# Kernel tuning notes

Hardware: AMD Instinct MI355X
Metric: run time of the kernel (lower is better)

Reference implementation:

```python
import jax, jax.numpy as jnp
import numpy as np

DIM = 96
HEADS = 4
HID = int(DIM * 2.66)  # 255, GDFN hidden width
B, H, W = 4, 128, 128


def _conv(x, w, b=None, groups=1):
    y = jax.lax.conv_general_dilated(x, w, (1, 1), 'SAME',
                                     dimension_numbers=('NCHW', 'OIHW', 'NCHW'),
                                     feature_group_count=groups)
    return y if b is None else y + b[None, :, None, None]


def _ln(x, w, b):
    # WithBias LayerNorm over channel dim (per pixel), biased variance, eps=1e-5
    mu = x.mean(1, keepdims=True)
    var = ((x - mu) ** 2).mean(1, keepdims=True)
    return (x - mu) / jnp.sqrt(var + 1e-5) * w[None, :, None, None] + b[None, :, None, None]


def _l2norm(x):
    # torch F.normalize(dim=-1): x / max(||x||_2, 1e-12)
    return x / jnp.maximum(jnp.linalg.norm(x, axis=-1, keepdims=True), 1e-12)


def _gelu(x):
    return jax.nn.gelu(x, approximate=False)


def setup_inputs() -> dict:
    key = jax.random.key(0)
    ks = iter(jax.random.split(key, 32))
    nrm = lambda shp, s=0.02: jax.random.normal(next(ks), shp, dtype=jnp.float32) * s
    d, h2 = DIM, HID
    inp = {
        'x': jax.random.normal(next(ks), (B, DIM, H, W), dtype=jnp.float32),
        # L_conv: 3x3(d->d,+b) GELU 1x1(d->1,+b)
        'Lc_w1': nrm((d, d, 3, 3)), 'Lc_b1': jnp.zeros((d,), jnp.float32),
        'Lc_w2': nrm((1, d, 1, 1)), 'Lc_b2': jnp.zeros((1,), jnp.float32),
        # R_conv: 3x3(d->d,+b) GELU 1x1(d->3,+b)
        'Rc_w1': nrm((d, d, 3, 3)), 'Rc_b1': jnp.zeros((d,), jnp.float32),
        'Rc_w2': nrm((3, d, 1, 1)), 'Rc_b2': jnp.zeros((3,), jnp.float32),
        # L_rein: 3x3(1->d,+b) GELU ; R_rein: 3x3(3->d,+b)
        'Lr_w': nrm((d, 1, 3, 3)), 'Lr_b': jnp.zeros((d,), jnp.float32),
        'Rr_w': nrm((d, 3, 3, 3)), 'Rr_b': jnp.zeros((d,), jnp.float32),
        # LayerNorms (WithBias)
        'n1_w': jnp.ones((d,), jnp.float32), 'n1_b': jnp.zeros((d,), jnp.float32),
        'nL_w': jnp.ones((d,), jnp.float32), 'nL_b': jnp.zeros((d,), jnp.float32),
        'n2_w': jnp.ones((d,), jnp.float32), 'n2_b': jnp.zeros((d,), jnp.float32),
        # Illum_Attention (bias=False)
        'temp': jnp.ones((HEADS, 1, 1), jnp.float32),
        'q_w': nrm((d, d, 1, 1)),
        'qd_w': nrm((d, d, 3, 3)),          # q_dwconv is a FULL 3x3 conv (no groups)
        'kv_w': nrm((2 * d, d, 1, 1)),
        'kvd_w': nrm((2 * d, 1, 3, 3)),     # depthwise, groups=2*dim
        'po_w': nrm((d, d, 1, 1)),
        # FeedForward (bias=False); NOTE: 'dwconv' here is a FULL 3x3 conv
        'pi_w': nrm((h2, d, 1, 1)),
        'fdw_w': nrm((h2, h2, 3, 3)),
        'fpo_w': nrm((d, h2, 1, 1)),
    }
    return inp


def reference(x, Lc_w1, Lc_b1, Lc_w2, Lc_b2, Rc_w1, Rc_b1, Rc_w2, Rc_b2,
              Lr_w, Lr_b, Rr_w, Rr_b, n1_w, n1_b, nL_w, nL_b, n2_w, n2_b,
              temp, q_w, qd_w, kv_w, kvd_w, po_w, pi_w, fdw_w, fpo_w):
    b, c, h, w = x.shape
    # Retinex decomposition heads
    L = _conv(_gelu(_conv(x, Lc_w1, Lc_b1)), Lc_w2, Lc_b2)   # [b,1,h,w]
    R = _conv(_gelu(_conv(x, Rc_w1, Rc_b1)), Rc_w2, Rc_b2)   # [b,3,h,w]
    L_rein = _gelu(_conv(jax.lax.stop_gradient(L), Lr_w, Lr_b))  # detach in torch
    R_rein = _conv(jax.lax.stop_gradient(R), Rr_w, Rr_b)
    # Illum_Guided_TransformerBlock: x = x + attn(norm1(x), normL(illum))
    xn = _ln(x, n1_w, n1_b)
    ill = _ln(L_rein, nL_w, nL_b)
    q = _conv(_conv(ill, q_w), qd_w)
    kv = _conv(_conv(xn, kv_w), kvd_w, groups=2 * c)
    k, v = jnp.split(kv, 2, axis=1)
    ch, hw = c // HEADS, h * w
    heads = lambda t: t.reshape(b, HEADS, ch, hw)
    qh, kh, vh = _l2norm(heads(q)), _l2norm(heads(k)), heads(v)
    # channel-wise attention: [b,heads,ch,ch]
    attn = jax.nn.softmax(jnp.einsum('bhci,bhdi->bhcd', qh, kh) * temp[None], axis=-1)
    out = jnp.einsum('bhcd,bhdi->bhci', attn, vh).reshape(b, c, h, w)
    x = x + _conv(out, po_w)
    # x = x + ffn(norm2(x))
    x2 = _ln(x, n2_w, n2_b)
    x = x + _conv(_gelu(_conv(_conv(x2, pi_w), fdw_w)), fpo_w)
    x = x + R_rein
    return (x, L, R)
```

## Files before the change

kernel.cpp:

```cpp
#include <hip/hip_runtime.h>

#define HWsz 16384
#define Wd 128

typedef unsigned short ushortT;
typedef unsigned int uintT;
typedef __attribute__((ext_vector_type(8))) short short8v;
typedef __attribute__((ext_vector_type(4))) float f32x4;
typedef __attribute__((ext_vector_type(16))) float f32x16;
typedef __attribute__((ext_vector_type(4))) unsigned short ushort4v;

__device__ __forceinline__ float gelu_f(float x){
    return 0.5f * x * (1.0f + erff(x * 0.70710678118654752f));
}
__device__ __forceinline__ ushortT f2b(float f){
    union { float f; uintT u; } v; v.f = f;
    uintT r = v.u + 0x7FFFu + ((v.u >> 16) & 1u);
    return (ushortT)(r >> 16);
}
__device__ __forceinline__ float b2f(ushortT u){
    union { uintT u; float f; } v; v.u = ((uintT)u) << 16; return v.f;
}

__device__ __forceinline__ void pack3_one(int e, const float* __restrict__ w,
    ushortT* __restrict__ outp, int cout, int cin, int BN, int NCH)
{
    int j = e & 7; int r = e >> 3;
    int ocl = r % BN; r /= BN;
    int kg  = r & 3;  r >>= 2;
    int tap = r % 9;  r /= 9;
    int ch  = r % NCH;
    int nt  = r / NCH;
    int ci = ch*32 + kg*8 + j;
    int oc = nt*BN + ocl;
    float v = (oc < cout && ci < cin) ? w[((size_t)oc*cin + ci)*9 + tap] : 0.f;
    outp[e] = f2b(v);
}
__device__ __forceinline__ void pack1_one(int e, const float* __restrict__ w,
    ushortT* __restrict__ outp, int cout, int cin, int BN, int NCH)
{
    int j = e & 7; int r = e >> 3;
    int ocl = r % BN; r /= BN;
    int kg  = r & 3;  r >>= 2;
    int ch  = r % NCH;
    int nt  = r / NCH;
    int ci = ch*32 + kg*8 + j;
    int oc = nt*BN + ocl;
    float v = (oc < cout && ci < cin) ? w[(size_t)oc*cin + ci] : 0.f;
    outp[e] = f2b(v);
}
__global__ __launch_bounds__(256) void pack_all_kernel(
    const float* Lc, const float* Rc, const float* Qd, const float* Fd,
    const float* Q1, const float* KV1, const float* PI1, const float* FPO1,
    ushortT* dL, ushortT* dR, ushortT* dQ, ushortT* dF,
    ushortT* dq0, ushortT* dkv, ushortT* dpi, ushortT* dfpo)
{
    int e = blockIdx.x*256 + threadIdx.x;
    if      (e < 82944)  pack3_one(e,        Lc, dL, 96, 96, 48, 3);
    else if (e < 165888) pack3_one(e-82944,  Rc, dR, 96, 96, 48, 3);
    else if (e < 248832) pack3_one(e-165888, Qd, dQ, 96, 96, 32, 3);
    else if (e < 838656) pack3_one(e-248832, Fd, dF, 255,255, 64, 8);
    else if (e < 847872) pack1_one(e-838656, Q1, dq0, 96, 96, 96, 3);
    else if (e < 866304) pack1_one(e-847872, KV1,dkv, 192,96, 48, 3);
    else if (e < 890880) pack1_one(e-866304, PI1,dpi, 255,96, 64, 3);
    else if (e < 915456) pack1_one(e-890880, FPO1,dfpo,96,255, 96, 8);
}

__global__ __launch_bounds__(256) void tonhwc_kernel(
    const float* __restrict__ in, ushortT* __restrict__ outp)
{
    const int p = blockIdx.x*256 + threadIdx.x;
    const int b = blockIdx.y;
    const float* ip = in + (size_t)b*96*HWsz + p;
    ushortT* op = outp + ((size_t)b*HWsz + p)*96;
#pragma unroll
    for (int g=0; g<12; g++){
        float v[8];
#pragma unroll
        for (int c=0;c<8;c++) v[c] = ip[(size_t)(g*8+c)*HWsz];
        uint4 pk;
        pk.x = (uintT)f2b(v[0]) | ((uintT)f2b(v[1])<<16);
        pk.y = (uintT)f2b(v[2]) | ((uintT)f2b(v[3])<<16);
        pk.z = (uintT)f2b(v[4]) | ((uintT)f2b(v[5])<<16);
        pk.w = (uintT)f2b(v[6]) | ((uintT)f2b(v[7])<<16);
        *(uint4*)(op + g*8) = pk;
    }
}

template<int NG, int NCH, int ACT, int TWOOUT>
__global__ __launch_bounds__(256,2) void conv3x3_v2(
    const ushortT* __restrict__ inh,
    const ushortT* __restrict__ wpk1, const ushortT* __restrict__ wpk2,
    const float* __restrict__ bias1, const float* __restrict__ bias2,
    ushortT* __restrict__ out1, ushortT* __restrict__ out2,
    int cout, int ocpad)
{
    constexpr int BN = NG*16;
    constexpr int Cpad = NCH*32;
    __shared__ __align__(16) ushortT As[4*180*8];

    const int tid = threadIdx.x;
    const int l   = tid & 63;
    const int wv  = tid >> 6;
    const int l15 = l & 15;
    const int kg  = l >> 4;
    const int tix = blockIdx.x & 7, tiy = blockIdx.x >> 3;
    const int b   = blockIdx.z;
    const int x0 = tix*16, y0 = tiy*8;

    const ushortT* wpk; const float* bias; ushortT* outp; int nt;
    if (TWOOUT){
        wpk  = (wv >= 2) ? wpk2 : wpk1;
        bias = (wv >= 2) ? bias2 : bias1;
        outp = (wv >= 2) ? out2 : out1;
        nt = wv & 1;
    } else { wpk = wpk1; bias = bias1; outp = out1; nt = wv; }
    const int ocbase = nt*BN;

    f32x4 acc[8][NG];
#pragma unroll
    for (int m=0;m<8;m++)
#pragma unroll
        for (int n=0;n<NG;n++) acc[m][n] = (f32x4){0.f,0.f,0.f,0.f};

    const ushortT* inb = inh + (size_t)b*HWsz*Cpad;

    for (int ch=0; ch<NCH; ch++){
        __syncthreads();
#pragma unroll
        for (int g=0; g<4; g++){
            int p = tid;
            if (p < 180){
                int hy = p/18, hx = p - hy*18;
                int gy = y0 + hy - 1, gx = x0 + hx - 1;
                uint4 v; v.x=0u; v.y=0u; v.z=0u; v.w=0u;
                if ((unsigned)gy < 128u && (unsigned)gx < 128u)
                    v = *(const uint4*)(inb + (size_t)(gy*Wd+gx)*Cpad + ch*32 + g*8);
                *(uint4*)(As + (g*180+p)*8) = v;
            }
        }
        __syncthreads();
        const ushortT* wch = wpk + (size_t)(nt*NCH + ch)*(9*4*BN*8);
#pragma unroll
        for (int tp=0; tp<9; tp++){
            const int dy = tp/3, dx = tp - dy*3;
            short8v bf[NG];
#pragma unroll
            for (int n=0;n<NG;n++)
                bf[n] = *(const short8v*)(wch + ((size_t)(tp*4 + kg)*BN + n*16 + l15)*8);
#pragma unroll
            for (int mg=0;mg<8;mg++){
                short8v a = *(const short8v*)(As + (kg*180 + (mg+dy)*18 + l15+dx)*8);
#pragma unroll
                for (int n=0;n<NG;n++)
                    acc[mg][n] = __builtin_amdgcn_mfma_f32_16x16x32_bf16(a, bf[n], acc[mg][n], 0,0,0);
            }
        }
    }
    __syncthreads();
    ushortT* Ts = As + wv*1024;
#pragma unroll
    for (int mg=0;mg<8;mg++){
        int gy = y0 + mg;
        ushortT* orow = outp + ((size_t)b*HWsz + gy*Wd + x0)*ocpad + ocbase;
#pragma unroll
        for (int n=0;n<NG;n++){
            int ocl = n*16 + l15;
            int oc  = ocbase + ocl;
            float bs = (bias && oc < cout) ? bias[oc] : 0.f;
#pragma unroll
            for (int j=0;j<4;j++){
                int pxj = kg*4 + j;
                float r = 0.f;
                if (oc < cout){ r = acc[mg][n][j] + bs; if (ACT) r = gelu_f(r); }
                int seg = ((ocl>>3) + pxj) & 7;
                Ts[pxj*64 + seg*8 + (ocl&7)] = f2b(r);
            }
        }
#pragma unroll
        for (int ps=0; ps < (BN+31)/32; ps++){
            int rpx = l & 15;
            int rs  = (l>>4) + ps*4;
            if (rs*8 < BN){
                int pseg = (rs + rpx) & 7;
                short8v v = *(const short8v*)(Ts + rpx*64 + pseg*8);
                *(short8v*)(orow + (size_t)rpx*ocpad + rs*8) = v;
            }
        }
    }
}

template<int NGW, int NCH>
__global__ __launch_bounds__(256) void gemm1x1_v2(
    const ushortT* __restrict__ inh, const ushortT* __restrict__ wpk,
    ushortT* __restrict__ outp, int cout, int ocpad)
{
    constexpr int BN = NGW*16;
    constexpr int Cpad = NCH*32;
    __shared__ __align__(16) ushortT Ts[4*16*64];

    const int tid = threadIdx.x;
    const int l = tid & 63, wv = tid >> 6, l15 = l & 15, kg = l >> 4;
    const int p0 = blockIdx.x*64;
    const int b  = blockIdx.z;
    const int nt = wv, ocbase = wv*BN;
    const ushortT* inb = inh + (size_t)b*HWsz*Cpad;

    f32x4 acc[4][NGW];
#pragma unroll
    for (int m=0;m<4;m++)
#pragma unroll
        for (int n=0;n<NGW;n++) acc[m][n] = (f32x4){0.f,0.f,0.f,0.f};

#pragma unroll
    for (int ch=0; ch<NCH; ch++){
        short8v a[4], bw[NGW];
#pragma unroll
        for (int mg=0; mg<4; mg++)
            a[mg] = *(const short8v*)(inb + (size_t)(p0 + mg*16 + l15)*Cpad + ch*32 + kg*8);
#pragma unroll
        for (int n=0;n<NGW;n++)
            bw[n] = *(const short8v*)(wpk + (((size_t)(nt*NCH + ch)*4 + kg)*BN + n*16 + l15)*8);
#pragma unroll
        for (int mg=0;mg<4;mg++)
#pragma unroll
            for (int n=0;n<NGW;n++)
                acc[mg][n] = __builtin_amdgcn_mfma_f32_16x16x32_bf16(a[mg], bw[n], acc[mg][n], 0,0,0);
    }
    ushortT* Tw = Ts + wv*1024;
#pragma unroll
    for (int mg=0;mg<4;mg++){
        ushortT* orow = outp + ((size_t)b*HWsz + p0 + mg*16)*ocpad + ocbase;
#pragma unroll
        for (int n=0;n<NGW;n++){
            int ocl = n*16 + l15;
            int oc  = ocbase + ocl;
#pragma unroll
            for (int j=0;j<4;j++){
                int pxj = kg*4 + j;
                float r = (oc < cout) ? acc[mg][n][j] : 0.f;
                int seg = ((ocl>>3) + pxj) & 7;
                Tw[pxj*64 + seg*8 + (ocl&7)] = f2b(r);
            }
        }
#pragma unroll
        for (int ps=0; ps < (BN+31)/32; ps++){
            int rpx = l & 15;
            int rs  = (l>>4) + ps*4;
            if (rs*8 < BN){
                int pseg = (rs + rpx) & 7;
                short8v v = *(const short8v*)(Tw + rpx*64 + pseg*8);
                *(short8v*)(orow + (size_t)rpx*ocpad + rs*8) = v;
            }
        }
    }
}

template<int NG, int NCH, int ACT, int OMODE, int NSPLIT, int XMAP>
__global__ __launch_bounds__(256,4) void conv3x3_mfma(
    const ushortT* __restrict__ inh,
    const ushortT* __restrict__ wpk1, const ushortT* __restrict__ wpk2,
    const float* __restrict__ bias1, const float* __restrict__ bias2,
    void* __restrict__ out1, void* __restrict__ out2,
    int cout, int ocpad)
{
    constexpr int BN = NG*16;
    constexpr int Cpad = NCH*32;
    __shared__ __align__(16) ushortT As[4*324*8];

    const int tid = threadIdx.x;
    const int l   = tid & 63;
    const int wv  = tid >> 6;
    const int l15 = l & 15;
    const int kg  = l >> 4;
    int tile = blockIdx.x, nt = blockIdx.y, b = blockIdx.z;
    const int tix = tile & 7, tiy = tile >> 3;

    const ushortT* wpk = wpk1; const float* bias = bias1; void* outv = out1;
    if (NSPLIT > 0 && nt >= NSPLIT){ nt -= NSPLIT; wpk = wpk2; bias = bias2; outv = out2; }

    f32x4 acc[4][NG];
#pragma unroll
    for (int m=0;m<4;m++)
#pragma unroll
        for (int n=0;n<NG;n++) acc[m][n] = (f32x4){0.f,0.f,0.f,0.f};

    const ushortT* inb = inh + (size_t)b*HWsz*Cpad;

    for (int ch=0; ch<NCH; ch++){
        __syncthreads();
#pragma unroll
        for (int g=0; g<4; g++){
            for (int p=tid; p<324; p+=256){
                int hy = p/18, hx = p - hy*18;
                int gy = tiy*16 + hy - 1, gx = tix*16 + hx - 1;
                uint4 v; v.x=0u; v.y=0u; v.z=0u; v.w=0u;
                if ((unsigned)gy < 128u && (unsigned)gx < 128u)
                    v = *(const uint4*)(inb + (size_t)(gy*Wd+gx)*Cpad + ch*32 + g*8);
                *(uint4*)(As + (g*324+p)*8) = v;
            }
        }
        __syncthreads();
        const ushortT* wch = wpk + (size_t)(nt*NCH + ch)*(9*4*BN*8);
#pragma unroll
        for (int tp=0; tp<9; tp++){
            const int dy = tp/3, dx = tp - dy*3;
            short8v a[4], bf[NG];
#pragma unroll
            for (int mg=0; mg<4; mg++){
                int p = (wv*4 + mg + dy)*18 + l15 + dx;
                a[mg] = *(const short8v*)(As + (kg*324 + p)*8);
            }
#pragma unroll
            for (int n=0;n<NG;n++)
                bf[n] = *(const short8v*)(wch + ((size_t)(tp*4 + kg)*BN + n*16 + l15)*8);
#pragma unroll
            for (int mg=0;mg<4;mg++)
#pragma unroll
                for (int n=0;n<NG;n++)
                    acc[mg][n] = __builtin_amdgcn_mfma_f32_16x16x32_bf16(a[mg], bf[n], acc[mg][n], 0,0,0);
        }
    }
    if (OMODE == 2){
        ushortT* out = (ushortT*)outv;
#pragma unroll
        for (int n=0;n<NG;n++){
            int oc = nt*BN + n*16 + l15;
            if (oc < cout){
                float bs = bias ? bias[oc] : 0.f;
#pragma unroll
                for (int mg=0;mg<4;mg++){
                    int gy = tiy*16 + wv*4 + mg;
                    int gx = tix*16 + kg*4;
                    ushort4v pk;
#pragma unroll
                    for (int j=0;j<4;j++){
                        float r = acc[mg][n][j] + bs;
                        if (ACT) r = gelu_f(r);
                        pk[j] = f2b(r);
                    }
                    *(ushort4v*)(out + ((size_t)b*cout + oc)*HWsz + gy*Wd + gx) = pk;
                }
            }
        }
    }
}

template<int NG, int NCH, int RES, int OMODE, int XMAP>
__global__ __launch_bounds__(256) void gemm1x1_mfma(
    const ushortT* __restrict__ inh, const ushortT* __restrict__ wpk, int wstride_z,
    const float* __restrict__ res1, const ushortT* __restrict__ res2b,
    void* __restrict__ outv, int cout, int ocpad)
{
    constexpr int BN = NG*16;
    constexpr int Cpad = NCH*32;
    constexpr int LSTR = (BN <= 64) ? 64 : 128;
    constexpr int MASK = LSTR/8 - 1;
    __shared__ __align__(16) ushortT TsS[(OMODE==1) ? 4*16*LSTR : 16];

    const int tid = threadIdx.x;
    const int l = tid & 63, wv = tid >> 6, l15 = l & 15, kg = l >> 4;
    int chunk = blockIdx.x, nt = blockIdx.y, b = blockIdx.z;
    const int p0 = chunk*256 + wv*64;
    const ushortT* inb = inh + (size_t)b*HWsz*Cpad;
    const ushortT* wp  = wpk + (size_t)b*wstride_z;

    f32x4 acc[4][NG];
#pragma unroll
    for (int m=0;m<4;m++)
#pragma unroll
        for (int n=0;n<NG;n++) acc[m][n] = (f32x4){0.f,0.f,0.f,0.f};

#pragma unroll
    for (int ch=0; ch<NCH; ch++){
        short8v a[4], bw[NG];
#pragma unroll
        for (int mg=0; mg<4; mg++)
            a[mg] = *(const short8v*)(inb + (size_t)(p0 + mg*16 + l15)*Cpad + ch*32 + kg*8);
#pragma unroll
        for (int n=0;n<NG;n++)
            bw[n] = *(const short8v*)(wp + (((size_t)(nt*NCH + ch)*4 + kg)*BN + n*16 + l15)*8);
#pragma unroll
        for (int mg=0;mg<4;mg++)
#pragma unroll
            for (int n=0;n<NG;n++)
                acc[mg][n] = __builtin_amdgcn_mfma_f32_16x16x32_bf16(a[mg], bw[n], acc[mg][n], 0,0,0);
    }
    if (OMODE == 0){
        float* out = (float*)outv;
#pragma unroll
        for (int n=0;n<NG;n++){
            int oc = nt*BN + n*16 + l15;
            if (oc < cout){
#pragma unroll
                for (int mg=0;mg<4;mg++){
                    int pix = p0 + mg*16 + kg*4;
                    size_t idx = ((size_t)b*cout + oc)*HWsz + pix;
                    float4 r;
                    r.x = acc[mg][n][0]; r.y = acc[mg][n][1];
                    r.z = acc[mg][n][2]; r.w = acc[mg][n][3];
                    if (RES>=1){ float4 q = *(const float4*)(res1+idx); r.x+=q.x;r.y+=q.y;r.z+=q.z;r.w+=q.w; }
                    if (RES>=2){
                        ushort4v q = *(const ushort4v*)(res2b+idx);
                        r.x+=b2f(q[0]); r.y+=b2f(q[1]); r.z+=b2f(q[2]); r.w+=b2f(q[3]);
                    }
                    *(float4*)(out + idx) = r;
                }
            }
        }
    } else {
        ushortT* outp = (ushortT*)outv;
        ushortT* Ts = TsS + wv*(16*LSTR);
#pragma unroll
        for (int mg=0;mg<4;mg++){
            ushortT* orow = outp + ((size_t)b*HWsz + p0 + mg*16)*ocpad + nt*BN;
#pragma unroll
            for (int n=0;n<NG;n++){
                int ocl = n*16 + l15;
                int oc  = nt*BN + ocl;
#pragma unroll
                for (int j=0;j<4;j++){
                    int pxj = kg*4 + j;
                    float r = (oc < cout) ? acc[mg][n][j] : 0.f;
                    int seg = ((ocl>>3) + pxj) & MASK;
                    Ts[pxj*LSTR + seg*8 + (ocl&7)] = f2b(r);
                }
            }
#pragma unroll
            for (int ps=0; ps < (BN+31)/32; ps++){
                int rpx = l & 15;
                int rs  = (l>>4) + ps*4;
                if (rs*8 < BN){
                    int pseg = (rs + rpx) & MASK;
                    short8v v = *(const short8v*)(Ts + rpx*LSTR + pseg*8);
                    *(short8v*)(orow + (size_t)rpx*ocpad + rs*8) = v;
                }
            }
        }
    }
}

template<int NOUT>
__global__ __launch_bounds__(256) void head1x1_kernel(
    const ushortT* __restrict__ inh, const float* __restrict__ w,
    const float* __restrict__ bias, float* __restrict__ out)
{
    __shared__ float lw[NOUT*96];
    const int tid = threadIdx.x;
    for (int t=tid; t<NOUT*96; t+=256) lw[t] = w[t];
    __syncthreads();
    const int p = blockIdx.x*256 + tid;
    const int b = blockIdx.y;
    const ushortT* ip = inh + ((size_t)b*HWsz + p)*96;
    float v[96];
#pragma unroll
    for (int g=0; g<12; g++){
        short8v s = *(const short8v*)(ip + g*8);
#pragma unroll
        for (int i=0;i<8;i++) v[g*8+i] = b2f((ushortT)s[i]);
    }
#pragma unroll
    for (int oc=0; oc<NOUT; oc++){
        float acc = bias[oc];
#pragma unroll
        for (int c=0;c<96;c++) acc += v[c]*lw[oc*96+c];
        out[((size_t)b*NOUT + oc)*HWsz + p] = acc;
    }
}

__global__ __launch_bounds__(256) void lrein_ln_kernel(
    const float* __restrict__ L, const float* __restrict__ w,
    const float* __restrict__ bias, const float* __restrict__ lnw,
    const float* __restrict__ lnb, ushortT* __restrict__ outh)
{
    __shared__ float sw[864], sb[96], sn1[96], sn2[96];
    const int tid = threadIdx.x;
    for (int t=tid; t<864; t+=256) sw[t] = w[t];
    if (tid < 96){ sb[tid]=bias[tid]; sn1[tid]=lnw[tid]; sn2[tid]=lnb[tid]; }
    __syncthreads();
    const int p = blockIdx.x*256 + tid;
    const int b = blockIdx.y;
    const int y = p>>7, x = p&127;
    const float* ib = L + (size_t)b*HWsz;
    float win[9];
#pragma unroll
    for (int dy=0;dy<3;dy++)
#pragma unroll
        for (int dx=0;dx<3;dx++){
            int gy=y+dy-1, gx=x+dx-1;
            win[dy*3+dx] = ((unsigned)gy<128u && (unsigned)gx<128u) ? ib[gy*Wd+gx] : 0.f;
        }
    float v[96]; float s=0.f;
#pragma unroll
    for (int c=0;c<96;c++){
        float a = sb[c];
#pragma unroll
        for (int t=0;t<9;t++) a += win[t]*sw[c*9+t];
        a = gelu_f(a);
        v[c]=a; s+=a;
    }
    const float mu = s*(1.f/96.f);
    float s2=0.f;
#pragma unroll
    for (int c=0;c<96;c++){ float d=v[c]-mu; s2+=d*d; }
    const float inv = 1.f/sqrtf(s2*(1.f/96.f)+1e-5f);
    ushortT* op = outh + ((size_t)b*HWsz + p)*96;
#pragma unroll
    for (int g=0; g<12; g++){
        uint4 pk; uintT w4[4];
#pragma unroll
        for (int i=0;i<4;i++){
            float r0 = (v[g*8+2*i]-mu)*inv*sn1[g*8+2*i]+sn2[g*8+2*i];
            float r1 = (v[g*8+2*i+1]-mu)*inv*sn1[g*8+2*i+1]+sn2[g*8+2*i+1];
            w4[i] = (uintT)f2b(r0) | ((uintT)f2b(r1)<<16);
        }
        pk.x=w4[0]; pk.y=w4[1]; pk.z=w4[2]; pk.w=w4[3];
        *(uint4*)(op + g*8) = pk;
    }
}

__global__ __launch_bounds__(256) void ln_n2n_kernel(
    const float* __restrict__ in, const float* __restrict__ w,
    const float* __restrict__ bias, ushortT* __restrict__ outh)
{
    const int p = blockIdx.x*256+threadIdx.x;
    const int b = blockIdx.y;
    const float* ip = in + (size_t)b*96*HWsz + p;
    float v[96]; float s=0.f;
#pragma unroll
    for(int c=0;c<96;c++){ v[c]=ip[(size_t)c*HWsz]; s+=v[c]; }
    const float mu = s*(1.f/96.f);
    float s2=0.f;
#pragma unroll
    for(int c=0;c<96;c++){ float d=v[c]-mu; s2+=d*d; }
    const float inv = 1.f/sqrtf(s2*(1.f/96.f)+1e-5f);
    ushortT* op = outh + ((size_t)b*HWsz + p)*96;
#pragma unroll
    for (int g=0; g<12; g++){
        uint4 pk; uintT w4[4];
#pragma unroll
        for (int i=0;i<4;i++){
            float r0 = (v[g*8+2*i]-mu)*inv*w[g*8+2*i]+bias[g*8+2*i];
            float r1 = (v[g*8+2*i+1]-mu)*inv*w[g*8+2*i+1]+bias[g*8+2*i+1];
            w4[i] = (uintT)f2b(r0) | ((uintT)f2b(r1)<<16);
        }
        pk.x=w4[0]; pk.y=w4[1]; pk.z=w4[2]; pk.w=w4[3];
        *(uint4*)(op + g*8) = pk;
    }
}

__global__ __launch_bounds__(256) void conv3x3_rr_kernel(
    const float* __restrict__ in, const float* __restrict__ w,
    const float* __restrict__ bias, ushortT* __restrict__ out)
{
    __shared__ float sw[216], sb[8];
    const int oc0 = blockIdx.y*8;
    if (threadIdx.x < 216) sw[threadIdx.x] = w[(size_t)oc0*27 + threadIdx.x];
    if (threadIdx.x < 8)   sb[threadIdx.x] = bias[oc0 + threadIdx.x];
    __syncthreads();
    const int p = blockIdx.x*256+threadIdx.x;
    const int b = blockIdx.z;
    const int y=p>>7, x=p&127;
    const float* ib = in + (size_t)b*3*HWsz;
    float win[27];
#pragma unroll
    for (int ci=0;ci<3;ci++)
#pragma unroll
        for (int dy=0;dy<3;dy++)
#pragma unroll
            for (int dx=0;dx<3;dx++){
                int gy=y+dy-1, gx=x+dx-1;
                win[ci*9+dy*3+dx] = ((unsigned)gy<128u && (unsigned)gx<128u)
                    ? ib[(size_t)ci*HWsz + gy*Wd+gx] : 0.f;
            }
#pragma unroll
    for (int i=0;i<8;i++){
        float acc = sb[i];
#pragma unroll
        for (int t=0;t<27;t++) acc += win[t]*sw[i*27+t];
        out[((size_t)b*96 + oc0+i)*HWsz + p] = f2b(acc);
    }
}

__global__ __launch_bounds__(256) void dw_nhwc_kernel(
    const ushortT* __restrict__ inh, const float* __restrict__ w,
    ushortT* __restrict__ kout, ushortT* __restrict__ vouth)
{
    const int p = blockIdx.x*256+threadIdx.x;
    const int c0 = blockIdx.y*8;
    const int b = blockIdx.z;
    const int y=p>>7, x=p&127;
    float lw[72];
#pragma unroll
    for (int i=0;i<8;i++)
#pragma unroll
        for (int t=0;t<9;t++) lw[i*9+t] = w[(size_t)(c0+i)*9 + t];
    const ushortT* ib = inh + (size_t)b*HWsz*192;
    float acc[8];
#pragma unroll
    for (int i=0;i<8;i++) acc[i]=0.f;
#pragma unroll
    for(int dy=0;dy<3;dy++){
        int gy=y+dy-1;
        if((unsigned)gy<128u){
#pragma unroll
            for(int dx=0;dx<3;dx++){
                int gx=x+dx-1;
                if((unsigned)gx<128u){
                    short8v s = *(const short8v*)(ib + (size_t)(gy*Wd+gx)*192 + c0);
#pragma unroll
                    for (int i=0;i<8;i++) acc[i] += b2f((ushortT)s[i])*lw[i*9+dy*3+dx];
                }
            }
        }
    }
    if (c0 < 96){
#pragma unroll
        for (int i=0;i<8;i++)
            kout[((size_t)b*96 + c0+i)*HWsz + p] = f2b(acc[i]);
    } else {
        ushortT* op = vouth + ((size_t)b*HWsz + p)*96 + (c0-96);
        uint4 pk;
        pk.x = (uintT)f2b(acc[0]) | ((uintT)f2b(acc[1])<<16);
        pk.y = (uintT)f2b(acc[2]) | ((uintT)f2b(acc[3])<<16);
        pk.z = (uintT)f2b(acc[4]) | ((uintT)f2b(acc[5])<<16);
        pk.w = (uintT)f2b(acc[6]) | ((uintT)f2b(acc[7])<<16);
        *(uint4*)op = pk;
    }
}

__global__ __launch_bounds__(256) void rownorm_bf16_kernel(
    const ushortT* __restrict__ qb, const ushortT* __restrict__ kb,
    float* __restrict__ invqk)
{
    __shared__ float red[256];
    const int r = blockIdx.x;
    const ushortT* ip = (r < 384) ? (qb + (size_t)r*HWsz) : (kb + (size_t)(r-384)*HWsz);
    float s=0.f;
    const ushortT* tp = ip + threadIdx.x*64;
#pragma unroll
    for (int g=0; g<8; g++){
        short8v v = *(const short8v*)(tp + g*8);
#pragma unroll
        for (int i=0;i<8;i++){ float f = b2f((ushortT)v[i]); s += f*f; }
    }
    red[threadIdx.x]=s; __syncthreads();
    for(int st=128; st>0; st>>=1){
        if(threadIdx.x<st) red[threadIdx.x]+=red[threadIdx.x+st];
        __syncthreads();
    }
    if(threadIdx.x==0) invqk[r] = 1.f/fmaxf(sqrtf(red[0]), 1e-12f);
}

__global__ __launch_bounds__(256) void qk_mfma_kernel(
    const ushortT* __restrict__ qb, const ushortT* __restrict__ kb,
    float* __restrict__ part)
{
    const int tid = threadIdx.x;
    const int l = tid & 63, wv = tid >> 6;
    const int chunk = blockIdx.x*4 + wv;
    const int bh = blockIdx.y, b = bh>>2, h = bh&3;
    const int ch = min(l & 31, 23);
    const int kh = (l >> 5)*8;
    const ushortT* qp = qb + ((size_t)b*96 + h*24 + ch)*HWsz + chunk*512 + kh;
    const ushortT* kp = kb + ((size_t)b*96 + h*24 + ch)*HWsz + chunk*512 + kh;
    f32x16 acc;
#pragma unroll
    for (int r=0;r<16;r++) acc[r]=0.f;
    for (int ks=0; ks<32; ks++){
        short8v a  = *(const short8v*)(qp + ks*16);
        short8v bb = *(const short8v*)(kp + ks*16);
        acc = __builtin_amdgcn_mfma_f32_32x32x16_bf16(a, bb, acc, 0,0,0);
    }
    float* op = part + ((size_t)chunk*16 + bh)*1024;
    const int col = l & 31;
#pragma unroll
    for (int r=0;r<16;r++){
        int row = (r&3) + 8*(r>>2) + 4*(l>>5);
        op[row*32 + col] = acc[r];
    }
}

__global__ void qk_reduce_kernel(const float* __restrict__ part, float* __restrict__ out)
{
    int idx = blockIdx.x*256+threadIdx.x;
    float s=0.f;
    for(int c=0;c<32;c++) s += part[(size_t)c*16384 + idx];
    out[idx]=s;
}

__global__ __launch_bounds__(576) void softmax_kernel(
    const float* __restrict__ raw, const float* __restrict__ invq,
    const float* __restrict__ invk, const float* __restrict__ temp,
    float* __restrict__ attn)
{
    __shared__ float l[576];
    const int bh=blockIdx.x, b=bh>>2, h=bh&3;
    const int tid=threadIdx.x;
    const int i=tid/24, j=tid-i*24;
    l[tid] = raw[(size_t)bh*1024 + i*32 + j] * invq[b*96+h*24+i] * invk[b*96+h*24+j] * temp[h];
    __syncthreads();
    if(tid<24){
        float m=-1e30f;
#pragma unroll
        for(int jj=0;jj<24;jj++) m = fmaxf(m, l[tid*24+jj]);
        float e[24]; float s=0.f;
#pragma unroll
        for(int jj=0;jj<24;jj++){ e[jj]=__expf(l[tid*24+jj]-m); s+=e[jj]; }
        float isv = 1.f/s;
#pragma unroll
        for(int jj=0;jj<24;jj++) attn[(size_t)bh*576 + tid*24 + jj] = e[jj]*isv;
    }
}

__global__ __launch_bounds__(256) void mkM_kernel(
    const float* __restrict__ attn, const float* __restrict__ po_w,
    ushortT* __restrict__ Mpk)
{
    const int b = blockIdx.x;
    for (int e = threadIdx.x; e < 9216; e += 256){
        int oc = e / 96, d = e - oc*96;
        int h = d / 24, dl = d - h*24;
        const float* aw = attn + ((size_t)(b*4+h))*576 + dl;
        const float* pw = po_w + (size_t)oc*96 + h*24;
        float s = 0.f;
#pragma unroll
        for (int c=0;c<24;c++) s += pw[c]*aw[c*24];
        int ch = d>>5, kg = (d>>3)&3, j = d&7;
        Mpk[(size_t)b*9216 + ((size_t)(ch*4+kg)*96 + oc)*8 + j] = f2b(s);
    }
}

extern "C" void kernel_launch(void* const* d_in, const int* in_sizes, int n_in,
                              void* d_out, int out_size, void* d_ws, size_t ws_size,
                              hipStream_t stream)
{
    const float* x     = (const float*)d_in[0];
    const float* Lc_w1 = (const float*)d_in[1];
    const float* Lc_b1 = (const float*)d_in[2];
    const float* Lc_w2 = (const float*)d_in[3];
    const float* Lc_b2 = (const float*)d_in[4];
    const float* Rc_w1 = (const float*)d_in[5];
    const float* Rc_b1 = (const float*)d_in[6];
    const float* Rc_w2 = (const float*)d_in[7];
    const float* Rc_b2 = (const float*)d_in[8];
    const float* Lr_w  = (const float*)d_in[9];
    const float* Lr_b  = (const float*)d_in[10];
    const float* Rr_w  = (const float*)d_in[11];
    const float* Rr_b  = (const float*)d_in[12];
    const float* n1_w  = (const float*)d_in[13];
    const float* n1_b  = (const float*)d_in[14];
    const float* nL_w  = (const float*)d_in[15];
    const float* nL_b  = (const float*)d_in[16];
    const float* n2_w  = (const float*)d_in[17];
    const float* n2_b  = (const float*)d_in[18];
    const float* temp  = (const float*)d_in[19];
    const float* q_w   = (const float*)d_in[20];
    const float* qd_w  = (const float*)d_in[21];
    const float* kv_w  = (const float*)d_in[22];
    const float* kvd_w = (const float*)d_in[23];
    const float* po_w  = (const float*)d_in[24];
    const float* pi_w  = (const float*)d_in[25];
    const float* fdw_w = (const float*)d_in[26];
    const float* fpo_w = (const float*)d_in[27];

    char* base = (char*)d_ws;
    ushortT* xh   = (ushortT*)(base + 0);
    ushortT* f0h  = (ushortT*)(base + 0);
    ushortT* Lh   = (ushortT*)(base + 33554432);
    ushortT* kv0h = (ushortT*)(base + 33554432);
    ushortT* f1h  = (ushortT*)(base + 33554432);
    ushortT* Rh   = (ushortT*)(base + 67108864);
    ushortT* vh   = (ushortT*)(base + 67108864);
    ushortT* x2nh = (ushortT*)(base + 67108864);
    ushortT* illh = (ushortT*)(base + 79691776);
    ushortT* xnh  = (ushortT*)(base + 92274688);
    ushortT* q0h  = (ushortT*)(base + 104857600);
    ushortT* qb   = (ushortT*)(base + 117440512);
    float*   x1   = (float*)(base + 117440512);
    ushortT* kb   = (ushortT*)(base + 142606336);
    ushortT* Bb   = (ushortT*)(base + 155189248);
    char* smb = base + 167772160;
    ushortT* wpkL = (ushortT*)smb;   smb += 165888;
    ushortT* wpkR = (ushortT*)smb;   smb += 165888;
    ushortT* wpkQ = (ushortT*)smb;   smb += 165888;
    ushortT* wpkF = (ushortT*)smb;   smb += 1179648;
    ushortT* wq0  = (ushortT*)smb;   smb += 18432;
    ushortT* wkv  = (ushortT*)smb;   smb += 36864;
    ushortT* wpi  = (ushortT*)smb;   smb += 49152;
    ushortT* wfpo = (ushortT*)smb;   smb += 49152;
    ushortT* Mpk  = (ushortT*)smb;   smb += 73728;
    float* invqk  = (float*)smb;     smb += 3072;
    float* part   = (float*)smb;     smb += 2097152;
    float* araw   = (float*)smb;     smb += 65536;
    float* attn   = (float*)smb;     smb += 36864;

    float* out_x = (float*)d_out;
    float* out_L = out_x + (size_t)4*96*HWsz;
    float* out_R = out_L + (size_t)4*HWsz;

    dim3 blk(256);

    hipLaunchKernelGGL(pack_all_kernel, dim3(3576), blk, 0, stream,
        Lc_w1, Rc_w1, qd_w, fdw_w, q_w, kv_w, pi_w, fpo_w,
        wpkL, wpkR, wpkQ, wpkF, wq0, wkv, wpi, wfpo);
    hipLaunchKernelGGL(tonhwc_kernel, dim3(64,4), blk, 0, stream, x, xh);

    hipLaunchKernelGGL((conv3x3_v2<3,3,1,1>), dim3(128,1,4), blk, 0, stream,
        xh, wpkL, wpkR, Lc_b1, Rc_b1, Lh, Rh, 96, 96);
    hipLaunchKernelGGL((head1x1_kernel<1>), dim3(64,4), blk, 0, stream, Lh, Lc_w2, Lc_b2, out_L);
    hipLaunchKernelGGL((head1x1_kernel<3>), dim3(64,4), blk, 0, stream, Rh, Rc_w2, Rc_b2, out_R);
    hipLaunchKernelGGL(lrein_ln_kernel, dim3(64,4), blk, 0, stream, out_L, Lr_w, Lr_b, nL_w, nL_b, illh);
    hipLaunchKernelGGL(conv3x3_rr_kernel, dim3(64,12,4), blk, 0, stream, out_R, Rr_w, Rr_b, Bb);

    hipLaunchKernelGGL(ln_n2n_kernel, dim3(64,4), blk, 0, stream, x, n1_w, n1_b, xnh);

    hipLaunchKernelGGL((gemm1x1_mfma<6,3,0,1,0>), dim3(64,1,4), blk, 0, stream,
        illh, wq0, 0, nullptr, nullptr, (void*)q0h, 96, 96);
    hipLaunchKernelGGL((conv3x3_mfma<2,3,0,2,0,0>), dim3(64,3,4), blk, 0, stream,
        q0h, wpkQ, wpkQ, nullptr, nullptr, (void*)qb, (void*)qb, 96, 0);
    hipLaunchKernelGGL((gemm1x1_v2<3,3>), dim3(256,1,4), blk, 0, stream,
        xnh, wkv, kv0h, 192, 192);
    hipLaunchKernelGGL(dw_nhwc_kernel, dim3(64,24,4), blk, 0, stream, kv0h, kvd_w, kb, vh);

    hipLaunchKernelGGL(rownorm_bf16_kernel, dim3(768), blk, 0, stream, qb, kb, invqk);
    hipLaunchKernelGGL(qk_mfma_kernel, dim3(8,16), blk, 0, stream, qb, kb, part);
    hipLaunchKernelGGL(qk_reduce_kernel, dim3(64), blk, 0, stream, part, araw);
    hipLaunchKernelGGL(softmax_kernel, dim3(16), dim3(576), 0, stream, araw, invqk, invqk+384, temp, attn);
    hipLaunchKernelGGL(mkM_kernel, dim3(4), blk, 0, stream, attn, po_w, Mpk);
    hipLaunchKernelGGL((gemm1x1_mfma<6,3,1,0,0>), dim3(64,1,4), blk, 0, stream,
        vh, Mpk, 9216, x, nullptr, (void*)x1, 96, 0);

    hipLaunchKernelGGL(ln_n2n_kernel, dim3(64,4), blk, 0, stream, x1, n2_w, n2_b, x2nh);
    hipLaunchKernelGGL((gemm1x1_v2<4,3>), dim3(256,1,4), blk, 0, stream,
        x2nh, wpi, f0h, 255, 256);
    hipLaunchKernelGGL((conv3x3_v2<4,8,1,0>), dim3(128,1,4), blk, 0, stream,
        f0h, wpkF, wpkF, nullptr, nullptr, f1h, f1h, 255, 256);
    hipLaunchKernelGGL((gemm1x1_mfma<6,8,2,0,0>), dim3(64,1,4), blk, 0, stream,
        f1h, wfpo, 0, x1, Bb, (void*)out_x, 96, 0);
}
```

Measured before the change: 408.1 us.

## Split 3x3 conv blocks by output-channel tile and stage weights in LDS

```diff
diff --git a/kernel.cpp b/kernel.cpp
--- a/kernel.cpp
+++ b/kernel.cpp
@@ -88,7 +88,7 @@
 }
 
 template<int NG, int NCH, int ACT, int TWOOUT>
-__global__ __launch_bounds__(256,2) void conv3x3_v2(
+__global__ __launch_bounds__(256,3) void conv3x3_v3(
     const ushortT* __restrict__ inh,
     const ushortT* __restrict__ wpk1, const ushortT* __restrict__ wpk2,
     const float* __restrict__ bias1, const float* __restrict__ bias2,
@@ -97,7 +97,9 @@
 {
     constexpr int BN = NG*16;
     constexpr int Cpad = NCH*32;
+    constexpr int WCH = 9*4*BN*8;
     __shared__ __align__(16) ushortT As[4*180*8];
+    __shared__ __align__(16) ushortT Ws[WCH];
 
     const int tid = threadIdx.x;
     const int l   = tid & 63;
@@ -108,18 +110,15 @@
     const int b   = blockIdx.z;
     const int x0 = tix*16, y0 = tiy*8;
 
-    const ushortT* wpk; const float* bias; ushortT* outp; int nt;
-    if (TWOOUT){
-        wpk  = (wv >= 2) ? wpk2 : wpk1;
-        bias = (wv >= 2) ? bias2 : bias1;
-        outp = (wv >= 2) ? out2 : out1;
-        nt = wv & 1;
-    } else { wpk = wpk1; bias = bias1; outp = out1; nt = wv; }
-    const int ocbase = nt*BN;
-
-    f32x4 acc[8][NG];
-#pragma unroll
-    for (int m=0;m<8;m++)
+    int nt = blockIdx.y;
+    const ushortT* wpk; const float* bias; ushortT* outp; int ntw;
+    if (TWOOUT && nt >= 2){ wpk = wpk2; bias = bias2; outp = out2; ntw = nt-2; }
+    else { wpk = wpk1; bias = bias1; outp = out1; ntw = nt; }
+    const int ocbase = ntw*BN;
+
+    f32x4 acc[2][NG];
+#pragma unroll
+    for (int m=0;m<2;m++)
 #pragma unroll
         for (int n=0;n<NG;n++) acc[m][n] = (f32x4){0.f,0.f,0.f,0.f};
 
@@ -127,30 +126,33 @@
 
     for (int ch=0; ch<NCH; ch++){
         __syncthreads();
-#pragma unroll
-        for (int g=0; g<4; g++){
-            int p = tid;
-            if (p < 180){
-                int hy = p/18, hx = p - hy*18;
-                int gy = y0 + hy - 1, gx = x0 + hx - 1;
+        if (tid < 180){
+            int hy = tid/18, hx = tid - hy*18;
+            int gy = y0 + hy - 1, gx = x0 + hx - 1;
+            bool ok = ((unsigned)gy < 128u) && ((unsigned)gx < 128u);
+#pragma unroll
+            for (int g=0; g<4; g++){
                 uint4 v; v.x=0u; v.y=0u; v.z=0u; v.w=0u;
-                if ((unsigned)gy < 128u && (unsigned)gx < 128u)
-                    v = *(const uint4*)(inb + (size_t)(gy*Wd+gx)*Cpad + ch*32 + g*8);
-                *(uint4*)(As + (g*180+p)*8) = v;
-            }
+                if (ok) v = *(const uint4*)(inb + (size_t)(gy*Wd+gx)*Cpad + ch*32 + g*8);
+                *(uint4*)(As + (g*180+tid)*8) = v;
+            }
+        }
+        {
+            const uint4* wsrc = (const uint4*)(wpk + ((size_t)ntw*NCH + ch)*WCH);
+            uint4* wdst = (uint4*)Ws;
+            for (int t=tid; t<WCH/8; t+=256) wdst[t] = wsrc[t];
         }
         __syncthreads();
-        const ushortT* wch = wpk + (size_t)(nt*NCH + ch)*(9*4*BN*8);
 #pragma unroll
         for (int tp=0; tp<9; tp++){
             const int dy = tp/3, dx = tp - dy*3;
             short8v bf[NG];
 #pragma unroll
             for (int n=0;n<NG;n++)
-                bf[n] = *(const short8v*)(wch + ((size_t)(tp*4 + kg)*BN + n*16 + l15)*8);
-#pragma unroll
-            for (int mg=0;mg<8;mg++){
-                short8v a = *(const short8v*)(As + (kg*180 + (mg+dy)*18 + l15+dx)*8);
+                bf[n] = *(const short8v*)(Ws + ((size_t)(tp*4 + kg)*BN + n*16 + l15)*8);
+#pragma unroll
+            for (int mg=0;mg<2;mg++){
+                short8v a = *(const short8v*)(As + (kg*180 + (wv*2+mg+dy)*18 + l15+dx)*8);
 #pragma unroll
                 for (int n=0;n<NG;n++)
                     acc[mg][n] = __builtin_amdgcn_mfma_f32_16x16x32_bf16(a, bf[n], acc[mg][n], 0,0,0);
@@ -160,8 +162,8 @@
     __syncthreads();
     ushortT* Ts = As + wv*1024;
 #pragma unroll
-    for (int mg=0;mg<8;mg++){
-        int gy = y0 + mg;
+    for (int mg=0;mg<2;mg++){
+        int gy = y0 + wv*2 + mg;
         ushortT* orow = outp + ((size_t)b*HWsz + gy*Wd + x0)*ocpad + ocbase;
 #pragma unroll
         for (int n=0;n<NG;n++){
@@ -806,7 +808,7 @@
         wpkL, wpkR, wpkQ, wpkF, wq0, wkv, wpi, wfpo);
     hipLaunchKernelGGL(tonhwc_kernel, dim3(64,4), blk, 0, stream, x, xh);
 
-    hipLaunchKernelGGL((conv3x3_v2<3,3,1,1>), dim3(128,1,4), blk, 0, stream,
+    hipLaunchKernelGGL((conv3x3_v3<3,3,1,1>), dim3(128,4,4), blk, 0, stream,
         xh, wpkL, wpkR, Lc_b1, Rc_b1, Lh, Rh, 96, 96);
     hipLaunchKernelGGL((head1x1_kernel<1>), dim3(64,4), blk, 0, stream, Lh, Lc_w2, Lc_b2, out_L);
     hipLaunchKernelGGL((head1x1_kernel<3>), dim3(64,4), blk, 0, stream, Rh, Rc_w2, Rc_b2, out_R);
@@ -834,7 +836,7 @@
     hipLaunchKernelGGL(ln_n2n_kernel, dim3(64,4), blk, 0, stream, x1, n2_w, n2_b, x2nh);
     hipLaunchKernelGGL((gemm1x1_v2<4,3>), dim3(256,1,4), blk, 0, stream,
         x2nh, wpi, f0h, 255, 256);
-    hipLaunchKernelGGL((conv3x3_v2<4,8,1,0>), dim3(128,1,4), blk, 0, stream,
+    hipLaunchKernelGGL((conv3x3_v3<4,8,1,0>), dim3(128,4,4), blk, 0, stream,
         f0h, wpkF, wpkF, nullptr, nullptr, f1h, f1h, 255, 256);
     hipLaunchKernelGGL((gemm1x1_mfma<6,8,2,0,0>), dim3(64,1,4), blk, 0, stream,
         f1h, wfpo, 0, x1, Bb, (void*)out_x, 96, 0);
```

Result: no change. 408.6 us (+0.1%).
